# Kernel optimization log

Measured on AMD Instinct MI355X. Metric: run time of the kernel, lower is better.

## Reference

```python
import jax, jax.numpy as jnp
import numpy as np

NUM_EXPERTS = 16
TOP_K = 2
D_IN = 1024
D_HID = 4096
D_OUT = 1024
BATCH = 8192


def setup_inputs() -> dict:
    key = jax.random.key(0)
    ks = jax.random.split(key, 6)
    s_in = 1.0 / np.sqrt(D_IN)
    s_hid = 1.0 / np.sqrt(D_HID)
    return {
        "x": jax.random.normal(ks[0], (BATCH, D_IN), dtype=jnp.float32),
        "Wg": jax.random.normal(ks[1], (D_IN, NUM_EXPERTS), dtype=jnp.float32) * s_in,
        "W1": jax.random.normal(ks[2], (NUM_EXPERTS, D_IN, D_HID), dtype=jnp.float32) * s_in,
        "b1": jnp.zeros((NUM_EXPERTS, D_HID), dtype=jnp.float32),
        "W2": jax.random.normal(ks[3], (NUM_EXPERTS, D_HID, D_OUT), dtype=jnp.float32) * s_hid,
        "b2": jnp.zeros((NUM_EXPERTS, D_OUT), dtype=jnp.float32),
    }


def _moe_forward(x, Wg, W1, b1, W2, b2):
    # Gating: top-k routing with softmax over the selected logits.
    logits = x @ Wg                                   # [B, E]
    top_vals, top_idx = jax.lax.top_k(logits, TOP_K)  # [B, k]
    routing_weights = jax.nn.softmax(top_vals, axis=-1)  # [B, k]

    # Per-token combine weight for each expert (sum over k slots):
    # cw[b, e] = sum_k routing_weights[b, k] * (top_idx[b, k] == e)
    one_hot = jax.nn.one_hot(top_idx, NUM_EXPERTS, dtype=x.dtype)  # [B, k, E]
    combine_w = jnp.einsum("bk,bke->be", routing_weights, one_hot)  # [B, E]

    # Per-expert MLP compute + weighted scatter-add combine.
    # Fixed-size loop over experts (structurally distinct weight slices);
    # equivalent math to the original's gather/compute/scatter dispatch.
    out = jnp.zeros((x.shape[0], D_OUT), dtype=x.dtype)
    for e in range(NUM_EXPERTS):
        h = jax.nn.relu(x @ W1[e] + b1[e])            # [B, H]
        y = h @ W2[e] + b2[e]                         # [B, O]
        out = out + combine_w[:, e:e + 1] * y
    return out


def reference(x, Wg, W1, b1, W2, b2):
    return _moe_forward(x, Wg, W1, b1, W2, b2)
```

## Files before the change

kernel.cpp:

```cpp
#include <hip/hip_runtime.h>
#include <cstdio>

#define DIN   1024
#define DHID  4096
#define DOUT  1024
#define NEXP  16
#define NTOK  8192
#define NPAIR (NTOK * 2)
#define PADMAX 20480
#define MAXTILES 80

typedef _Float16 h8 __attribute__((ext_vector_type(8)));
typedef _Float16 h4 __attribute__((ext_vector_type(4)));
typedef float    f4 __attribute__((ext_vector_type(4)));

#define C_CNT  0
#define C_POFF 16
#define C_CUR  32
#define C_NT   48
#define C_TE   64
#define C_TP   256

__device__ __forceinline__ void async16(const void* g, void* l) {
  __builtin_amdgcn_global_load_lds((const __attribute__((address_space(1))) void*)g,
                                   (__attribute__((address_space(3))) void*)l, 16, 0, 0);
}

__global__ void k_init(float* __restrict__ out, const float* __restrict__ x,
                       _Float16* __restrict__ x16, int* __restrict__ ptok,
                       float* __restrict__ pw, int* __restrict__ ctrl) {
  int i = blockIdx.x * 256 + threadIdx.x;
  ((f4*)out)[i] = (f4){0.f, 0.f, 0.f, 0.f};
  float4 v = ((const float4*)x)[i];
  h4 hv = {(_Float16)v.x, (_Float16)v.y, (_Float16)v.z, (_Float16)v.w};
  ((h4*)x16)[i] = hv;
  if (i < PADMAX) { ptok[i] = 0; pw[i] = 0.f; }
  if (i < 1024) ctrl[i] = 0;
}

__global__ void k_gate(const float* __restrict__ x, const float* __restrict__ wg,
                       int* __restrict__ te, float* __restrict__ tw,
                       int* __restrict__ ctrl) {
  int t = blockIdx.x * 4 + (threadIdx.x >> 6);
  int l = threadIdx.x & 63;
  const float* xr = x + (long)t * DIN;
  float acc[NEXP];
#pragma unroll
  for (int e = 0; e < NEXP; ++e) acc[e] = 0.f;
  for (int k = l; k < DIN; k += 64) {
    float xv = xr[k];
    const float4* wr = (const float4*)(wg + (long)k * NEXP);
    float4 a = wr[0], b = wr[1], c = wr[2], d = wr[3];
    acc[0]  += xv * a.x; acc[1]  += xv * a.y; acc[2]  += xv * a.z; acc[3]  += xv * a.w;
    acc[4]  += xv * b.x; acc[5]  += xv * b.y; acc[6]  += xv * b.z; acc[7]  += xv * b.w;
    acc[8]  += xv * c.x; acc[9]  += xv * c.y; acc[10] += xv * c.z; acc[11] += xv * c.w;
    acc[12] += xv * d.x; acc[13] += xv * d.y; acc[14] += xv * d.z; acc[15] += xv * d.w;
  }
#pragma unroll
  for (int off = 32; off > 0; off >>= 1) {
#pragma unroll
    for (int e = 0; e < NEXP; ++e) acc[e] += __shfl_xor(acc[e], off, 64);
  }
  if (l == 0) {
    float v0 = -1e30f; int e0 = 0;
#pragma unroll
    for (int e = 0; e < NEXP; ++e) if (acc[e] > v0) { v0 = acc[e]; e0 = e; }
    float v1 = -1e30f; int e1 = 0;
#pragma unroll
    for (int e = 0; e < NEXP; ++e) if (e != e0 && acc[e] > v1) { v1 = acc[e]; e1 = e; }
    float d = expf(v1 - v0);
    float den = 1.f / (1.f + d);
    te[2 * t] = e0;     tw[2 * t] = den;
    te[2 * t + 1] = e1; tw[2 * t + 1] = d * den;
    atomicAdd(&ctrl[C_CNT + e0], 1);
    atomicAdd(&ctrl[C_CNT + e1], 1);
  }
}

__global__ void k_scan(int* __restrict__ ctrl) {
  __shared__ int sOff[NEXP], sT0[NEXP], sTiles[NEXP];
  int tid = threadIdx.x;
  if (tid == 0) {
    int off = 0, nt = 0;
    for (int e = 0; e < NEXP; ++e) {
      int c = ctrl[C_CNT + e];
      int tiles = (c + 255) >> 8;
      ctrl[C_POFF + e] = off;
      ctrl[C_CUR + e] = off;
      sOff[e] = off; sT0[e] = nt; sTiles[e] = tiles;
      nt += tiles;
      off += tiles * 256;
    }
    ctrl[C_NT] = nt;
  }
  __syncthreads();
  int nt = sT0[NEXP - 1] + sTiles[NEXP - 1];
  for (int j = tid; j < nt; j += blockDim.x) {
    int e = 0;
#pragma unroll
    for (int k = 1; k < NEXP; ++k) if (j >= sT0[k]) e = k;
    ctrl[C_TE + j] = e;
    ctrl[C_TP + j] = sOff[e] + (j - sT0[e]) * 256;
  }
}

__global__ void k_assign(const int* __restrict__ te, const float* __restrict__ tw,
                         int* __restrict__ ctrl, int* __restrict__ ptok,
                         float* __restrict__ pw) {
  int t = blockIdx.x * 256 + threadIdx.x;
#pragma unroll
  for (int s = 0; s < 2; ++s) {
    int e = te[2 * t + s];
    int pos = atomicAdd(&ctrl[C_CUR + e], 1);
    ptok[pos] = t;
    pw[pos] = tw[2 * t + s];
  }
}

__global__ void k_transpose(const float* __restrict__ W, _Float16* __restrict__ out,
                            int R, int C) {
  __shared__ __align__(16) _Float16 tile[64][136];
  int e = blockIdx.z;
  const float* Wb = W + ((long)e * R + blockIdx.x * 128) * C + blockIdx.y * 64;
  int tid = threadIdx.x;
  int rr = tid >> 4;
  int cc = (tid & 15) * 4;
#pragma unroll
  for (int i = 0; i < 8; ++i) {
    int r = rr + i * 16;
    float4 v = *(const float4*)(Wb + (long)r * C + cc);
    tile[cc + 0][r] = (_Float16)v.x;
    tile[cc + 1][r] = (_Float16)v.y;
    tile[cc + 2][r] = (_Float16)v.z;
    tile[cc + 3][r] = (_Float16)v.w;
  }
  __syncthreads();
  _Float16* ob = out + ((long)e * C + blockIdx.y * 64) * R + blockIdx.x * 128;
  int c2 = tid >> 4;
  int ch = tid & 15;
#pragma unroll
  for (int i = 0; i < 4; ++i) {
    int c = c2 + i * 16;
    *(h8*)(ob + (long)c * R + ch * 8) = *(const h8*)&tile[c][ch * 8];
  }
}

template<int KD, int ND, int G1, int KP>
__global__ __launch_bounds__(512, 2)
void k_gemm(const _Float16* __restrict__ A, const _Float16* __restrict__ Wt,
            const float* __restrict__ bias, const int* __restrict__ ctrl,
            const int* __restrict__ ptok, const float* __restrict__ pw,
            _Float16* __restrict__ Hout, float* __restrict__ out) {
  __shared__ __align__(16) _Float16 sm[65536];

  constexpr int NW = (ND / 256) * KP * MAXTILES;
  constexpr int QX = NW / 8;
  int bid = blockIdx.x;
  int wid = (bid & 7) * QX + (bid >> 3);
  int mt = wid % MAXTILES;
  int g  = wid / MAXTILES;
  int kp = (KP > 1) ? (g % KP) : 0;
  int nb = g / KP;

  if (mt >= ctrl[C_NT]) return;
  int e  = ctrl[C_TE + mt];
  int p0 = ctrl[C_TP + mt];
  int n0 = nb * 256;
  long kbase = (long)kp * (KD / KP);
  int tid = threadIdx.x;
  int w = tid >> 6, l = tid & 63;
  int wm = w & 1, wn = w >> 1;
  int ln15 = l & 15, lq = l >> 4;

  const _Float16* agp[4];
  const _Float16* bgp[4];
#pragma unroll
  for (int h = 0; h < 2; ++h)
#pragma unroll
    for (int j = 0; j < 2; ++j) {
      int r = (w * 2 + j) * 8 + (l >> 3);
      int c = (l & 7) ^ (r & 7);
      long arow = G1 ? (long)ptok[p0 + h * 128 + r] : (long)(p0 + h * 128 + r);
      agp[h * 2 + j] = A + arow * KD + kbase + c * 8;
      bgp[h * 2 + j] = Wt + ((long)e * ND + n0 + h * 128 + r) * KD + kbase + c * 8;
    }

  auto stageH = [&](int t, int half) {
    _Float16* dst = sm + (t & 1) * 32768 + (half & 1) * 16384 + (half >> 1) * 8192
                    + w * 1024;
    long koff = (long)t * 64;
    const _Float16* const* gp = (half & 1) ? bgp : agp;
#pragma unroll
    for (int j = 0; j < 2; ++j)
      async16(gp[(half >> 1) * 2 + j] + koff, dst + j * 512);
  };

  f4 acc[2][4][2][2];
#pragma unroll
  for (int mq = 0; mq < 2; ++mq)
#pragma unroll
    for (int i = 0; i < 4; ++i)
#pragma unroll
      for (int nq = 0; nq < 2; ++nq)
#pragma unroll
        for (int j = 0; j < 2; ++j) acc[mq][i][nq][j] = (f4){0.f, 0.f, 0.f, 0.f};

  h8 af[8], bf0[4], bf1[4];

  auto readA = [&](int d, int mq) {
    const _Float16* Ab = sm + d * 32768 + mq * 8192;
#pragma unroll
    for (int i = 0; i < 4; ++i) {
      int rh = wm * 64 + i * 16 + ln15;
#pragma unroll
      for (int ks = 0; ks < 2; ++ks)
        af[i * 2 + ks] = *(const h8*)&Ab[rh * 64 + (((ks * 4 + lq)) ^ (rh & 7)) * 8];
    }
  };
  auto readB = [&](int d, int nq, h8* bf) {
    const _Float16* Bb = sm + d * 32768 + 16384 + nq * 8192;
#pragma unroll
    for (int j = 0; j < 2; ++j) {
      int rh = wn * 32 + j * 16 + ln15;
#pragma unroll
      for (int ks = 0; ks < 2; ++ks)
        bf[j * 2 + ks] = *(const h8*)&Bb[rh * 64 + (((ks * 4 + lq)) ^ (rh & 7)) * 8];
    }
  };
  auto mfmaQ = [&](int mq, int nq, const h8* bf) {
    __builtin_amdgcn_s_setprio(1);
#pragma unroll
    for (int ks = 0; ks < 2; ++ks)
#pragma unroll
      for (int i = 0; i < 4; ++i)
#pragma unroll
        for (int j = 0; j < 2; ++j)
          acc[mq][i][nq][j] = __builtin_amdgcn_mfma_f32_16x16x32_f16(
              af[i * 2 + ks], bf[j * 2 + ks], acc[mq][i][nq][j], 0, 0, 0);
    __builtin_amdgcn_s_setprio(0);
  };

  constexpr int KSTEPS = KD / 64 / KP;

  stageH(0, 0); stageH(0, 1); stageH(0, 2); stageH(0, 3);
  stageH(1, 0); stageH(1, 1); stageH(1, 2);
  asm volatile("s_waitcnt vmcnt(6)" ::: "memory");
  __builtin_amdgcn_s_barrier();

#pragma unroll 2
  for (int t = 0; t < KSTEPS; ++t) {
    int d = t & 1;
    readA(d, 0);
    readB(d, 0, bf0);
    if (t + 1 < KSTEPS) stageH(t + 1, 3);
    __builtin_amdgcn_s_barrier();
    asm volatile("s_waitcnt lgkmcnt(0)" ::: "memory");
    mfmaQ(0, 0, bf0);
    __builtin_amdgcn_s_barrier();
    readB(d, 1, bf1);
    if (t + 2 < KSTEPS) stageH(t + 2, 0);
    __builtin_amdgcn_s_barrier();
    asm volatile("s_waitcnt lgkmcnt(0)" ::: "memory");
    mfmaQ(0, 1, bf1);
    __builtin_amdgcn_s_barrier();
    readA(d, 1);
    if (t + 2 < KSTEPS) stageH(t + 2, 1);
    __builtin_amdgcn_s_barrier();
    asm volatile("s_waitcnt lgkmcnt(0)" ::: "memory");
    mfmaQ(1, 1, bf1);
    __builtin_amdgcn_s_barrier();
    if (t + 2 < KSTEPS) stageH(t + 2, 2);
    if (t + 1 < KSTEPS) {
      if (t + 2 < KSTEPS) asm volatile("s_waitcnt vmcnt(6)" ::: "memory");
      else                asm volatile("s_waitcnt vmcnt(0)" ::: "memory");
    }
    __builtin_amdgcn_s_barrier();
    mfmaQ(1, 0, bf0);
    __builtin_amdgcn_s_barrier();
  }

  float bj[2][2];
#pragma unroll
  for (int nq = 0; nq < 2; ++nq)
#pragma unroll
    for (int j = 0; j < 2; ++j)
      bj[nq][j] = bias[e * ND + n0 + nq * 128 + wn * 32 + j * 16 + ln15];
  if (KP > 1 && kp != 0) {
#pragma unroll
    for (int nq = 0; nq < 2; ++nq)
#pragma unroll
      for (int j = 0; j < 2; ++j) bj[nq][j] = 0.f;
  }

  if (G1) {
    _Float16* cs = sm;
#pragma unroll
    for (int mq = 0; mq < 2; ++mq) {
      if (mq) __syncthreads();
#pragma unroll
      for (int i = 0; i < 4; ++i)
#pragma unroll
        for (int reg = 0; reg < 4; ++reg) {
          int row = wm * 64 + i * 16 + lq * 4 + reg;
#pragma unroll
          for (int nq = 0; nq < 2; ++nq)
#pragma unroll
            for (int j = 0; j < 2; ++j)
              cs[row * 264 + nq * 128 + wn * 32 + j * 16 + ln15] =
                  (_Float16)fmaxf(acc[mq][i][nq][j][reg] + bj[nq][j], 0.f);
        }
      __syncthreads();
#pragma unroll
      for (int p = 0; p < 8; ++p) {
        int idx = p * 512 + tid;
        int row = idx >> 5, ch = idx & 31;
        *(h8*)(Hout + (long)(p0 + mq * 128 + row) * DHID + n0 + ch * 8) =
            *(const h8*)&cs[row * 264 + ch * 8];
      }
    }
  } else {
#pragma unroll
    for (int mq = 0; mq < 2; ++mq)
#pragma unroll
      for (int i = 0; i < 4; ++i)
#pragma unroll
        for (int reg = 0; reg < 4; ++reg) {
          int p = p0 + mq * 128 + wm * 64 + i * 16 + lq * 4 + reg;
          float wgt = pw[p];
          if (wgt != 0.f) {
            int tk = ptok[p];
            float* orow = out + (long)tk * DOUT + n0;
#pragma unroll
            for (int nq = 0; nq < 2; ++nq)
#pragma unroll
              for (int j = 0; j < 2; ++j)
                atomicAdd(&orow[nq * 128 + wn * 32 + j * 16 + ln15],
                          wgt * (acc[mq][i][nq][j][reg] + bj[nq][j]));
          }
        }
  }
}

extern "C" void kernel_launch(void* const* d_in, const int* in_sizes, int n_in,
                              void* d_out, int out_size, void* d_ws, size_t ws_size,
                              hipStream_t stream) {
  const float* x  = (const float*)d_in[0];
  const float* Wg = (const float*)d_in[1];
  const float* W1 = (const float*)d_in[2];
  const float* b1 = (const float*)d_in[3];
  const float* W2 = (const float*)d_in[4];
  const float* b2 = (const float*)d_in[5];
  float* out = (float*)d_out;
  char* ws = (char*)d_ws;

  size_t WT_OFF = 0;
  size_t H_OFF  = WT_OFF + (size_t)NEXP * DHID * DIN * 2;
  size_t X_OFF  = H_OFF  + (size_t)PADMAX * DHID * 2;
  size_t TE_OFF = X_OFF  + (size_t)NTOK * DIN * 2;
  size_t TW_OFF = TE_OFF + (size_t)NPAIR * 4;
  size_t PT_OFF = TW_OFF + (size_t)NPAIR * 4;
  size_t PW_OFF = PT_OFF + (size_t)PADMAX * 4;
  size_t CT_OFF = PW_OFF + (size_t)PADMAX * 4;
  size_t END    = CT_OFF + 4096;
  if (ws_size < END) {
    fprintf(stderr, "kernel_launch: ws too small (%zu < %zu)\n", ws_size, END);
    return;
  }
  _Float16* Wt  = (_Float16*)(ws + WT_OFF);
  _Float16* H   = (_Float16*)(ws + H_OFF);
  _Float16* x16 = (_Float16*)(ws + X_OFF);
  int*   te   = (int*)(ws + TE_OFF);
  float* tw   = (float*)(ws + TW_OFF);
  int*   pt   = (int*)(ws + PT_OFF);
  float* pw   = (float*)(ws + PW_OFF);
  int*   ctrl = (int*)(ws + CT_OFF);

  k_init<<<NTOK * DIN / (256 * 4), 256, 0, stream>>>(out, x, x16, pt, pw, ctrl);
  k_gate<<<NTOK / 4, 256, 0, stream>>>(x, Wg, te, tw, ctrl);
  k_scan<<<1, 256, 0, stream>>>(ctrl);
  k_assign<<<NTOK / 256, 256, 0, stream>>>(te, tw, ctrl, pt, pw);

  k_transpose<<<dim3(DIN / 128, DHID / 64, NEXP), 256, 0, stream>>>(W1, Wt, DIN, DHID);
  k_gemm<DIN, DHID, 1, 1><<<dim3((DHID / 256) * MAXTILES), 512, 0, stream>>>(
      x16, Wt, b1, ctrl, pt, pw, H, nullptr);

  k_transpose<<<dim3(DHID / 128, DOUT / 64, NEXP), 256, 0, stream>>>(W2, Wt, DHID, DOUT);
  k_gemm<DHID, DOUT, 0, 4><<<dim3((DOUT / 256) * 4 * MAXTILES), 512, 0, stream>>>(
      H, Wt, b2, ctrl, pt, pw, nullptr, out);
}
```

Before: 1.357 ms.

## Fuse fp32 weight transpose/convert into GEMM B-tile staging, drop split-K

Removes the separate k_transpose passes that converted W1/W2 from fp32 to transposed fp16 in workspace. Each GEMM now loads fp32 weight tiles straight into registers, converts them to fp16 and writes them into swizzled LDS inside the pipelined K loop. The second GEMM also drops its 4-way split-K, so fewer blocks launch, each running the full K=4096 loop. This avoids a large extra read and write of all expert weights, but doubles the global bytes per B tile, adds register pressure and conversion work inside the main loop, and lowers parallelism in GEMM2.

```diff
diff --git a/kernel.cpp b/kernel.cpp
--- a/kernel.cpp
+++ b/kernel.cpp
@@ -117,63 +117,31 @@
   }
 }
 
-__global__ void k_transpose(const float* __restrict__ W, _Float16* __restrict__ out,
-                            int R, int C) {
-  __shared__ __align__(16) _Float16 tile[64][136];
-  int e = blockIdx.z;
-  const float* Wb = W + ((long)e * R + blockIdx.x * 128) * C + blockIdx.y * 64;
-  int tid = threadIdx.x;
-  int rr = tid >> 4;
-  int cc = (tid & 15) * 4;
-#pragma unroll
-  for (int i = 0; i < 8; ++i) {
-    int r = rr + i * 16;
-    float4 v = *(const float4*)(Wb + (long)r * C + cc);
-    tile[cc + 0][r] = (_Float16)v.x;
-    tile[cc + 1][r] = (_Float16)v.y;
-    tile[cc + 2][r] = (_Float16)v.z;
-    tile[cc + 3][r] = (_Float16)v.w;
-  }
-  __syncthreads();
-  _Float16* ob = out + ((long)e * C + blockIdx.y * 64) * R + blockIdx.x * 128;
-  int c2 = tid >> 4;
-  int ch = tid & 15;
-#pragma unroll
-  for (int i = 0; i < 4; ++i) {
-    int c = c2 + i * 16;
-    *(h8*)(ob + (long)c * R + ch * 8) = *(const h8*)&tile[c][ch * 8];
-  }
-}
-
-template<int KD, int ND, int G1, int KP>
+template<int KD, int ND, int G1>
 __global__ __launch_bounds__(512, 2)
-void k_gemm(const _Float16* __restrict__ A, const _Float16* __restrict__ Wt,
+void k_gemm(const _Float16* __restrict__ A, const float* __restrict__ W,
             const float* __restrict__ bias, const int* __restrict__ ctrl,
             const int* __restrict__ ptok, const float* __restrict__ pw,
             _Float16* __restrict__ Hout, float* __restrict__ out) {
   __shared__ __align__(16) _Float16 sm[65536];
 
-  constexpr int NW = (ND / 256) * KP * MAXTILES;
-  constexpr int QX = NW / 8;
+  constexpr int NWK = (ND / 256) * MAXTILES;
+  constexpr int QX = NWK / 8;
   int bid = blockIdx.x;
   int wid = (bid & 7) * QX + (bid >> 3);
   int mt = wid % MAXTILES;
-  int g  = wid / MAXTILES;
-  int kp = (KP > 1) ? (g % KP) : 0;
-  int nb = g / KP;
+  int nb = wid / MAXTILES;
 
   if (mt >= ctrl[C_NT]) return;
   int e  = ctrl[C_TE + mt];
   int p0 = ctrl[C_TP + mt];
   int n0 = nb * 256;
-  long kbase = (long)kp * (KD / KP);
   int tid = threadIdx.x;
   int w = tid >> 6, l = tid & 63;
   int wm = w & 1, wn = w >> 1;
   int ln15 = l & 15, lq = l >> 4;
 
   const _Float16* agp[4];
-  const _Float16* bgp[4];
 #pragma unroll
   for (int h = 0; h < 2; ++h)
 #pragma unroll
@@ -181,18 +149,48 @@
       int r = (w * 2 + j) * 8 + (l >> 3);
       int c = (l & 7) ^ (r & 7);
       long arow = G1 ? (long)ptok[p0 + h * 128 + r] : (long)(p0 + h * 128 + r);
-      agp[h * 2 + j] = A + arow * KD + kbase + c * 8;
-      bgp[h * 2 + j] = Wt + ((long)e * ND + n0 + h * 128 + r) * KD + kbase + c * 8;
-    }
-
-  auto stageH = [&](int t, int half) {
-    _Float16* dst = sm + (t & 1) * 32768 + (half & 1) * 16384 + (half >> 1) * 8192
-                    + w * 1024;
+      agp[h * 2 + j] = A + arow * KD + c * 8;
+    }
+  auto stageA = [&](int t, int h) {
+    _Float16* dst = sm + (t & 1) * 32768 + h * 8192 + w * 1024;
     long koff = (long)t * 64;
-    const _Float16* const* gp = (half & 1) ? bgp : agp;
-#pragma unroll
-    for (int j = 0; j < 2; ++j)
-      async16(gp[(half >> 1) * 2 + j] + koff, dst + j * 512);
+    async16(agp[h * 2 + 0] + koff, dst);
+    async16(agp[h * 2 + 1] + koff, dst + 512);
+  };
+
+  int kb  = (w & 3) * 4 + lq;
+  int nq4 = (l & 15) + (w >> 2) * 16;
+  const float* gB0 = W + ((long)e * KD + kb * 4) * ND + n0 + nq4 * 4;
+  const float* gB1 = gB0 + 128;
+  int bwo[2][4];
+#pragma unroll
+  for (int it = 0; it < 2; ++it)
+#pragma unroll
+    for (int j = 0; j < 4; ++j) {
+      int r = (nq4 + it * 32) * 4 + j;
+      bwo[it][j] = 16384 + (r >> 7) * 8192 + (r & 127) * 64
+                 + (((kb >> 1) ^ (r & 7)) << 3) + (kb & 1) * 4;
+    }
+  f4 breg[8];
+  auto loadB = [&](int t) {
+    const float* pa = gB0 + (long)t * 64 * ND;
+    const float* pb = gB1 + (long)t * 64 * ND;
+#pragma unroll
+    for (int i = 0; i < 4; ++i) {
+      breg[i]     = *(const f4*)(pa + (long)i * ND);
+      breg[4 + i] = *(const f4*)(pb + (long)i * ND);
+    }
+  };
+  auto writeB = [&](int t) {
+    _Float16* dstb = sm + (t & 1) * 32768;
+#pragma unroll
+    for (int it = 0; it < 2; ++it)
+#pragma unroll
+      for (int j = 0; j < 4; ++j) {
+        h4 hv = {(_Float16)breg[it * 4 + 0][j], (_Float16)breg[it * 4 + 1][j],
+                 (_Float16)breg[it * 4 + 2][j], (_Float16)breg[it * 4 + 3][j]};
+        *(h4*)&dstb[bwo[it][j]] = hv;
+      }
   };
 
   f4 acc[2][4][2][2];
@@ -240,11 +238,15 @@
     __builtin_amdgcn_s_setprio(0);
   };
 
-  constexpr int KSTEPS = KD / 64 / KP;
-
-  stageH(0, 0); stageH(0, 1); stageH(0, 2); stageH(0, 3);
-  stageH(1, 0); stageH(1, 1); stageH(1, 2);
-  asm volatile("s_waitcnt vmcnt(6)" ::: "memory");
+  constexpr int KSTEPS = KD / 64;
+
+  loadB(0);
+  stageA(0, 0); stageA(0, 1); stageA(1, 0); stageA(1, 1);
+  asm volatile("s_waitcnt vmcnt(8)" ::: "memory");
+  writeB(0);
+  loadB(1);
+  asm volatile("s_waitcnt vmcnt(12)" ::: "memory");
+  asm volatile("s_waitcnt lgkmcnt(0)" ::: "memory");
   __builtin_amdgcn_s_barrier();
 
 #pragma unroll 2
@@ -252,27 +254,28 @@
     int d = t & 1;
     readA(d, 0);
     readB(d, 0, bf0);
-    if (t + 1 < KSTEPS) stageH(t + 1, 3);
     __builtin_amdgcn_s_barrier();
     asm volatile("s_waitcnt lgkmcnt(0)" ::: "memory");
     mfmaQ(0, 0, bf0);
     __builtin_amdgcn_s_barrier();
     readB(d, 1, bf1);
-    if (t + 2 < KSTEPS) stageH(t + 2, 0);
+    if (t + 2 < KSTEPS) stageA(t + 2, 0);
     __builtin_amdgcn_s_barrier();
     asm volatile("s_waitcnt lgkmcnt(0)" ::: "memory");
     mfmaQ(0, 1, bf1);
     __builtin_amdgcn_s_barrier();
     readA(d, 1);
-    if (t + 2 < KSTEPS) stageH(t + 2, 1);
     __builtin_amdgcn_s_barrier();
     asm volatile("s_waitcnt lgkmcnt(0)" ::: "memory");
     mfmaQ(1, 1, bf1);
     __builtin_amdgcn_s_barrier();
-    if (t + 2 < KSTEPS) stageH(t + 2, 2);
+    if (t + 2 < KSTEPS) stageA(t + 2, 1);
     if (t + 1 < KSTEPS) {
-      if (t + 2 < KSTEPS) asm volatile("s_waitcnt vmcnt(6)" ::: "memory");
+      if (t + 2 < KSTEPS) asm volatile("s_waitcnt vmcnt(4)" ::: "memory");
       else                asm volatile("s_waitcnt vmcnt(0)" ::: "memory");
+      writeB(t + 1);
+      if (t + 2 < KSTEPS) loadB(t + 2);
+      asm volatile("s_waitcnt lgkmcnt(0)" ::: "memory");
     }
     __builtin_amdgcn_s_barrier();
     mfmaQ(1, 0, bf0);
@@ -285,12 +288,6 @@
 #pragma unroll
     for (int j = 0; j < 2; ++j)
       bj[nq][j] = bias[e * ND + n0 + nq * 128 + wn * 32 + j * 16 + ln15];
-  if (KP > 1 && kp != 0) {
-#pragma unroll
-    for (int nq = 0; nq < 2; ++nq)
-#pragma unroll
-      for (int j = 0; j < 2; ++j) bj[nq][j] = 0.f;
-  }
 
   if (G1) {
     _Float16* cs = sm;
@@ -353,8 +350,7 @@
   float* out = (float*)d_out;
   char* ws = (char*)d_ws;
 
-  size_t WT_OFF = 0;
-  size_t H_OFF  = WT_OFF + (size_t)NEXP * DHID * DIN * 2;
+  size_t H_OFF  = 0;
   size_t X_OFF  = H_OFF  + (size_t)PADMAX * DHID * 2;
   size_t TE_OFF = X_OFF  + (size_t)NTOK * DIN * 2;
   size_t TW_OFF = TE_OFF + (size_t)NPAIR * 4;
@@ -366,7 +362,6 @@
     fprintf(stderr, "kernel_launch: ws too small (%zu < %zu)\n", ws_size, END);
     return;
   }
-  _Float16* Wt  = (_Float16*)(ws + WT_OFF);
   _Float16* H   = (_Float16*)(ws + H_OFF);
   _Float16* x16 = (_Float16*)(ws + X_OFF);
   int*   te   = (int*)(ws + TE_OFF);
@@ -380,11 +375,9 @@
   k_scan<<<1, 256, 0, stream>>>(ctrl);
   k_assign<<<NTOK / 256, 256, 0, stream>>>(te, tw, ctrl, pt, pw);
 
-  k_transpose<<<dim3(DIN / 128, DHID / 64, NEXP), 256, 0, stream>>>(W1, Wt, DIN, DHID);
-  k_gemm<DIN, DHID, 1, 1><<<dim3((DHID / 256) * MAXTILES), 512, 0, stream>>>(
-      x16, Wt, b1, ctrl, pt, pw, H, nullptr);
-
-  k_transpose<<<dim3(DHID / 128, DOUT / 64, NEXP), 256, 0, stream>>>(W2, Wt, DHID, DOUT);
-  k_gemm<DHID, DOUT, 0, 4><<<dim3((DOUT / 256) * 4 * MAXTILES), 512, 0, stream>>>(
-      H, Wt, b2, ctrl, pt, pw, nullptr, out);
-}
+  k_gemm<DIN, DHID, 1><<<dim3((DHID / 256) * MAXTILES), 512, 0, stream>>>(
+      x16, W1, b1, ctrl, pt, pw, H, nullptr);
+
+  k_gemm<DHID, DOUT, 0><<<dim3((DOUT / 256) * MAXTILES), 512, 0, stream>>>(
+      H, W2, b2, ctrl, pt, pw, nullptr, out);
+}
```

Result: slower. 1.870 ms (+37.9%).

## Replace weight transpose with k-blocked fp16 layout and reorder GEMM tile mapping

Applied to the files above, without the earlier changes.

Replaces the shared-memory transpose kernel with a grid-stride prep kernel that stores weights as [E][K/8][N][8] fp16 blocks, so the conversion reads coalesced along N without a transpose tile. The GEMM B-operand addressing is changed to match this layout, with each k-step advancing by 64*ND elements. The block-to-work mapping now makes N-blocks and k-splits vary fastest within an M tile, which should improve reuse of the gathered A rows. The second GEMM's split-K factor drops from 4 to 2, giving fewer atomic output partials but less parallelism. The B loads now stride across N rows in 16-byte chunks, which may hurt global access coalescing.

```diff
diff --git a/kernel.cpp b/kernel.cpp
--- a/kernel.cpp
+++ b/kernel.cpp
@@ -117,31 +117,20 @@
   }
 }
 
-__global__ void k_transpose(const float* __restrict__ W, _Float16* __restrict__ out,
-                            int R, int C) {
-  __shared__ __align__(16) _Float16 tile[64][136];
-  int e = blockIdx.z;
-  const float* Wb = W + ((long)e * R + blockIdx.x * 128) * C + blockIdx.y * 64;
-  int tid = threadIdx.x;
-  int rr = tid >> 4;
-  int cc = (tid & 15) * 4;
-#pragma unroll
-  for (int i = 0; i < 8; ++i) {
-    int r = rr + i * 16;
-    float4 v = *(const float4*)(Wb + (long)r * C + cc);
-    tile[cc + 0][r] = (_Float16)v.x;
-    tile[cc + 1][r] = (_Float16)v.y;
-    tile[cc + 2][r] = (_Float16)v.z;
-    tile[cc + 3][r] = (_Float16)v.w;
-  }
-  __syncthreads();
-  _Float16* ob = out + ((long)e * C + blockIdx.y * 64) * R + blockIdx.x * 128;
-  int c2 = tid >> 4;
-  int ch = tid & 15;
-#pragma unroll
-  for (int i = 0; i < 4; ++i) {
-    int c = c2 + i * 16;
-    *(h8*)(ob + (long)c * R + ch * 8) = *(const h8*)&tile[c][ch * 8];
+__global__ void k_wprep(const float* __restrict__ W, _Float16* __restrict__ Wt,
+                        int KD, int ND) {
+  int KO = KD >> 3;
+  long total = (long)NEXP * KO * ND;
+  long stride = (long)gridDim.x * blockDim.x;
+  for (long it = (long)blockIdx.x * blockDim.x + threadIdx.x; it < total; it += stride) {
+    long n  = it & (ND - 1);
+    long ko = (it / ND) & (KO - 1);
+    long e  = it / ((long)ND * KO);
+    const float* src = W + (e * KD + ko * 8) * ND + n;
+    h8 v;
+#pragma unroll
+    for (int kk = 0; kk < 8; ++kk) v[kk] = (_Float16)src[(long)kk * ND];
+    *(h8*)(Wt + it * 8) = v;
   }
 }
 
@@ -153,20 +142,22 @@
             _Float16* __restrict__ Hout, float* __restrict__ out) {
   __shared__ __align__(16) _Float16 sm[65536];
 
-  constexpr int NW = (ND / 256) * KP * MAXTILES;
+  constexpr int NB = ND / 256;
+  constexpr int KO = KD / 8;
+  constexpr int NW = NB * KP * MAXTILES;
   constexpr int QX = NW / 8;
   int bid = blockIdx.x;
   int wid = (bid & 7) * QX + (bid >> 3);
-  int mt = wid % MAXTILES;
-  int g  = wid / MAXTILES;
-  int kp = (KP > 1) ? (g % KP) : 0;
-  int nb = g / KP;
+  int g  = wid % (NB * KP);
+  int mt = wid / (NB * KP);
+  int nb = g % NB;
+  int kp = g / NB;
 
   if (mt >= ctrl[C_NT]) return;
   int e  = ctrl[C_TE + mt];
   int p0 = ctrl[C_TP + mt];
   int n0 = nb * 256;
-  long kbase = (long)kp * (KD / KP);
+  int kbase = kp * (KD / KP);
   int tid = threadIdx.x;
   int w = tid >> 6, l = tid & 63;
   int wm = w & 1, wn = w >> 1;
@@ -182,17 +173,22 @@
       int c = (l & 7) ^ (r & 7);
       long arow = G1 ? (long)ptok[p0 + h * 128 + r] : (long)(p0 + h * 128 + r);
       agp[h * 2 + j] = A + arow * KD + kbase + c * 8;
-      bgp[h * 2 + j] = Wt + ((long)e * ND + n0 + h * 128 + r) * KD + kbase + c * 8;
+      bgp[h * 2 + j] = Wt + (((long)e * KO + kbase / 8 + c) * ND
+                             + (n0 + h * 128 + r)) * 8;
     }
 
   auto stageH = [&](int t, int half) {
     _Float16* dst = sm + (t & 1) * 32768 + (half & 1) * 16384 + (half >> 1) * 8192
                     + w * 1024;
-    long koff = (long)t * 64;
-    const _Float16* const* gp = (half & 1) ? bgp : agp;
-#pragma unroll
-    for (int j = 0; j < 2; ++j)
-      async16(gp[(half >> 1) * 2 + j] + koff, dst + j * 512);
+    if (half & 1) {
+      long koff = (long)t * 64 * ND;
+      async16(bgp[(half >> 1) * 2 + 0] + koff, dst);
+      async16(bgp[(half >> 1) * 2 + 1] + koff, dst + 512);
+    } else {
+      long koff = (long)t * 64;
+      async16(agp[(half >> 1) * 2 + 0] + koff, dst);
+      async16(agp[(half >> 1) * 2 + 1] + koff, dst + 512);
+    }
   };
 
   f4 acc[2][4][2][2];
@@ -380,11 +376,11 @@
   k_scan<<<1, 256, 0, stream>>>(ctrl);
   k_assign<<<NTOK / 256, 256, 0, stream>>>(te, tw, ctrl, pt, pw);
 
-  k_transpose<<<dim3(DIN / 128, DHID / 64, NEXP), 256, 0, stream>>>(W1, Wt, DIN, DHID);
+  k_wprep<<<4096, 256, 0, stream>>>(W1, Wt, DIN, DHID);
   k_gemm<DIN, DHID, 1, 1><<<dim3((DHID / 256) * MAXTILES), 512, 0, stream>>>(
       x16, Wt, b1, ctrl, pt, pw, H, nullptr);
 
-  k_transpose<<<dim3(DHID / 128, DOUT / 64, NEXP), 256, 0, stream>>>(W2, Wt, DHID, DOUT);
-  k_gemm<DHID, DOUT, 0, 4><<<dim3((DOUT / 256) * 4 * MAXTILES), 512, 0, stream>>>(
+  k_wprep<<<4096, 256, 0, stream>>>(W2, Wt, DHID, DOUT);
+  k_gemm<DHID, DOUT, 0, 2><<<dim3((DOUT / 256) * 2 * MAXTILES), 512, 0, stream>>>(
       H, Wt, b2, ctrl, pt, pw, nullptr, out);
 }
```

After: 1.296 ms. -4.4%, faster.
